# Optimization experiments

Hardware: AMD Instinct MI355X
Metric: run time of the kernel (lower is better)

The kernel has to match this reference:

```python
import jax, jax.numpy as jnp
import numpy as np

NHEAD = 8

def setup_inputs() -> dict:
    key = jax.random.key(0)
    k1, k2, k3, k4 = jax.random.split(key, 4)
    B, N, I, KQ, V = 2, 4096, 512, 512, 512
    x = jax.random.normal(k1, (B, N, I), dtype=jnp.float32)
    # store weights as [in, out] so projection is x @ W (same math as torch Linear with W.T)
    Wk = jax.random.normal(k2, (I, KQ), dtype=jnp.float32) * (1.0 / np.sqrt(I))
    Wq = jax.random.normal(k3, (I, KQ), dtype=jnp.float32) * (1.0 / np.sqrt(I))
    Wv = jax.random.normal(k4, (I, V), dtype=jnp.float32) * (1.0 / np.sqrt(I))
    return {"x": x, "Wk": Wk, "Wq": Wq, "Wv": Wv}

def reference(x, Wk, Wq, Wv):
    B, N, _ = x.shape
    H = NHEAD
    k = (x @ Wk).reshape(B, N, H, -1)   # [B,N,H,dk]
    q = (x @ Wq).reshape(B, N, H, -1)   # [B,N,H,dk]
    v = (x @ Wv).reshape(B, N, H, -1)   # [B,N,H,dv]
    dk = k.shape[-1]
    # scores[b,n,m,h] = k[b,n,h,:] . q[b,m,h,:] / sqrt(dk)
    scores = jnp.einsum('bnhd,bmhd->bnmh', k, q) / jnp.sqrt(jnp.asarray(dk, x.dtype))
    attn = jax.nn.softmax(scores, axis=-2)  # softmax over m (dim -2), matching torch code
    out = jnp.einsum('bnmh,bmhd->bnhd', attn, v)
    return out.reshape(B, N, -1)
```

## Files before the change

kernel.cpp:

```cpp
#include <hip/hip_runtime.h>
#include <hip/hip_bf16.h>

typedef __bf16 bf16_t;
typedef bf16_t bf16x8 __attribute__((ext_vector_type(8)));
typedef bf16_t bf16x4 __attribute__((ext_vector_type(4)));
typedef float f32x4 __attribute__((ext_vector_type(4)));

#define MFMA16(a, b, c) __builtin_amdgcn_mfma_f32_16x16x32_bf16(a, b, c, 0, 0, 0)

typedef __attribute__((address_space(3))) unsigned int lds_u32_t;
typedef __attribute__((address_space(1))) const unsigned int glb_u32_t;

__device__ __forceinline__ void gload16(const void* g, void* l) {
    __builtin_amdgcn_global_load_lds((glb_u32_t*)g, (lds_u32_t*)l, 16, 0, 0);
}

__device__ __forceinline__ bf16x8 lds8(const bf16_t* base, int row, int cb) {
    return *reinterpret_cast<const bf16x8*>(
        reinterpret_cast<const char*>(base) + row * 128 + (cb ^ ((row & 7) << 4)));
}

__global__ __launch_bounds__(256) void convert_x(
    const float* __restrict__ X, bf16_t* __restrict__ Xb)
{
    const size_t i = ((size_t)blockIdx.x * 256 + threadIdx.x) * 8;
    const float4 v0 = *reinterpret_cast<const float4*>(&X[i]);
    const float4 v1 = *reinterpret_cast<const float4*>(&X[i + 4]);
    bf16x8 o;
    o[0] = (bf16_t)v0.x; o[1] = (bf16_t)v0.y; o[2] = (bf16_t)v0.z; o[3] = (bf16_t)v0.w;
    o[4] = (bf16_t)v1.x; o[5] = (bf16_t)v1.y; o[6] = (bf16_t)v1.z; o[7] = (bf16_t)v1.w;
    *reinterpret_cast<bf16x8*>(&Xb[i]) = o;
}

__global__ __launch_bounds__(256) void transpose_w(
    const float* __restrict__ Wq, const float* __restrict__ Wk,
    const float* __restrict__ Wv, bf16_t* __restrict__ Wt)
{
    __shared__ float T[64][65];
    const int mat = blockIdx.z;
    const float* W = (mat == 0) ? Wq : (mat == 1 ? Wk : Wv);
    const int k0 = blockIdx.x * 64, n0 = blockIdx.y * 64;
    const int r = threadIdx.x >> 4, c4 = (threadIdx.x & 15) * 4;

    for (int rep = 0; rep < 4; ++rep) {
        const int row = r + rep * 16;
        const float4 v = *reinterpret_cast<const float4*>(&W[(size_t)(k0 + row) * 512 + n0 + c4]);
        T[row][c4 + 0] = v.x; T[row][c4 + 1] = v.y;
        T[row][c4 + 2] = v.z; T[row][c4 + 3] = v.w;
    }
    __syncthreads();
    const float scl = (mat == 1) ? 0.1803368801111204f : 1.0f;
    for (int rep = 0; rep < 4; ++rep) {
        const int nrow = r + rep * 16;
        bf16x4 o;
        for (int e = 0; e < 4; ++e) o[e] = (bf16_t)(T[c4 + e][nrow] * scl);
        *reinterpret_cast<bf16x4*>(&Wt[(size_t)mat * 262144 + (size_t)(n0 + nrow) * 512 + k0 + c4]) = o;
    }
}

__global__ __launch_bounds__(256, 2) void proj_bf16(
    const bf16_t* __restrict__ Xb, const bf16_t* __restrict__ Wt,
    bf16_t* __restrict__ Qb, bf16_t* __restrict__ Kb, bf16_t* __restrict__ Vt)
{
    __shared__ bf16_t Ab[2][128 * 64];
    __shared__ bf16_t Bb[2][128 * 64];

    const int tid = threadIdx.x;
    const int w = tid >> 6, l = tid & 63, g = l >> 4, lr = l & 15;
    const int m0 = blockIdx.x * 128;
    const int mat = blockIdx.y >> 2;
    const int n0 = (blockIdx.y & 3) * 128;
    const bf16_t* Wm = Wt + (size_t)mat * 262144;
    const int wm = (w >> 1) * 64, wn = (w & 1) * 64;

#define STAGE_P(buf, k0v)                                                   \
    do {                                                                    \
        for (int t = 0; t < 4; ++t) {                                       \
            const int rb = w * 32 + t * 8;                                  \
            const int row = rb + (l >> 3);                                  \
            const int cb = ((l & 7) << 4) ^ ((row & 7) << 4);               \
            gload16(&Xb[(size_t)(m0 + row) * 512 + (k0v) + (cb >> 1)],      \
                    &Ab[buf][rb * 64]);                                     \
            gload16(&Wm[(size_t)(n0 + row) * 512 + (k0v) + (cb >> 1)],      \
                    &Bb[buf][rb * 64]);                                     \
        }                                                                   \
    } while (0)

    f32x4 acc[4][4];
    const f32x4 z4 = {0.f, 0.f, 0.f, 0.f};
#pragma unroll
    for (int i = 0; i < 4; ++i)
#pragma unroll
        for (int j = 0; j < 4; ++j) acc[i][j] = z4;

    STAGE_P(0, 0);
    __syncthreads();

    for (int kk = 0; kk < 8; ++kk) {
        const int cur = kk & 1;
        if (kk + 1 < 8) STAGE_P(cur ^ 1, (kk + 1) * 64);

        bf16x8 a[4][2], bq[4][2];
#pragma unroll
        for (int fa = 0; fa < 4; ++fa)
#pragma unroll
            for (int dh = 0; dh < 2; ++dh) {
                a[fa][dh]  = lds8(Ab[cur], wm + fa * 16 + lr, dh * 64 + g * 16);
                bq[fa][dh] = lds8(Bb[cur], wn + fa * 16 + lr, dh * 64 + g * 16);
            }
        __builtin_amdgcn_s_setprio(1);
#pragma unroll
        for (int fa = 0; fa < 4; ++fa)
#pragma unroll
            for (int fb = 0; fb < 4; ++fb) {
                acc[fa][fb] = MFMA16(a[fa][0], bq[fb][0], acc[fa][fb]);
                acc[fa][fb] = MFMA16(a[fa][1], bq[fb][1], acc[fa][fb]);
            }
        __builtin_amdgcn_s_setprio(0);
        __syncthreads();
    }
#undef STAGE_P

#pragma unroll
    for (int fa = 0; fa < 4; ++fa)
#pragma unroll
        for (int fb = 0; fb < 4; ++fb)
#pragma unroll
            for (int j = 0; j < 4; ++j) {
                const int m = m0 + wm + fa * 16 + g * 4 + j;
                const int n = n0 + wn + fb * 16 + lr;
                const bf16_t val = (bf16_t)acc[fa][fb][j];
                if (mat == 0) {
                    Qb[(size_t)m * 512 + n] = val;
                } else if (mat == 1) {
                    Kb[(size_t)m * 512 + n] = val;
                } else {
                    const int b_ = m >> 12, mm = m & 4095;
                    const int hh = n >> 6, d = n & 63;
                    const int loc = mm & 63;
                    const int mperm = (mm & ~63) | (loc & 32) |
                                      (((loc >> 2) & 3) << 3) |
                                      (((loc >> 4) & 1) << 2) | (loc & 3);
                    Vt[((size_t)((b_ * 8 + hh) * 64 + d)) * 4096 + mperm] = val;
                }
            }
}

__global__ __launch_bounds__(256) void proj_kernel(
    const float* __restrict__ X,
    const float* __restrict__ Wq, const float* __restrict__ Wk,
    const float* __restrict__ Wv,
    bf16_t* __restrict__ Qb, bf16_t* __restrict__ Kb, bf16_t* __restrict__ Vt)
{
    __shared__ bf16_t Ax[128][40];
    __shared__ bf16_t Wtl[64][40];

    const int mode = blockIdx.z;
    const float* W = (mode == 0) ? Wq : (mode == 1 ? Wk : Wv);
    bf16_t* C = (mode == 0) ? Qb : (mode == 1 ? Kb : Vt);

    const int tid = threadIdx.x;
    const int w = tid >> 6, l = tid & 63, g = l >> 4, lr = l & 15;
    const int m0 = blockIdx.x * 128, n0 = blockIdx.y * 64;

    f32x4 acc[2][4];
    const f32x4 z4 = {0.f, 0.f, 0.f, 0.f};
    for (int i = 0; i < 2; ++i)
        for (int j = 0; j < 4; ++j) acc[i][j] = z4;

    for (int k0 = 0; k0 < 512; k0 += 32) {
        {
            const int c4 = (tid & 7) * 4;
            for (int r = 0; r < 4; ++r) {
                const int row = (tid >> 3) + r * 32;
                const float4 v = *reinterpret_cast<const float4*>(
                    &X[(size_t)(m0 + row) * 512 + k0 + c4]);
                bf16x4 o;
                o[0] = (bf16_t)v.x; o[1] = (bf16_t)v.y;
                o[2] = (bf16_t)v.z; o[3] = (bf16_t)v.w;
                *reinterpret_cast<bf16x4*>(&Ax[row][c4]) = o;
            }
        }
        {
            const int c4 = (tid & 15) * 4;
            for (int r = 0; r < 2; ++r) {
                const int krow = (tid >> 4) + r * 16;
                const float4 v = *reinterpret_cast<const float4*>(
                    &W[(size_t)(k0 + krow) * 512 + n0 + c4]);
                Wtl[c4 + 0][krow] = (bf16_t)v.x;
                Wtl[c4 + 1][krow] = (bf16_t)v.y;
                Wtl[c4 + 2][krow] = (bf16_t)v.z;
                Wtl[c4 + 3][krow] = (bf16_t)v.w;
            }
        }
        __syncthreads();

        bf16x8 a[2], bq[4];
        for (int fr = 0; fr < 2; ++fr)
            a[fr] = *reinterpret_cast<const bf16x8*>(&Ax[w * 32 + fr * 16 + lr][g * 8]);
        for (int fn = 0; fn < 4; ++fn)
            bq[fn] = *reinterpret_cast<const bf16x8*>(&Wtl[fn * 16 + lr][g * 8]);
        for (int fr = 0; fr < 2; ++fr)
            for (int fn = 0; fn < 4; ++fn)
                acc[fr][fn] = MFMA16(a[fr], bq[fn], acc[fr][fn]);
        __syncthreads();
    }

    const float SCL = 0.125f * 1.44269504088896f;
    for (int fr = 0; fr < 2; ++fr)
        for (int fn = 0; fn < 4; ++fn)
            for (int j = 0; j < 4; ++j) {
                const int m = m0 + w * 32 + fr * 16 + g * 4 + j;
                const int n = n0 + fn * 16 + lr;
                float vf = acc[fr][fn][j];
                if (mode == 1) vf *= SCL;
                const bf16_t val = (bf16_t)vf;
                if (mode <= 1) {
                    C[(size_t)m * 512 + n] = val;
                } else {
                    const int b_ = m >> 12, mm = m & 4095;
                    const int hh = n >> 6, d = n & 63;
                    const int loc = mm & 63;
                    const int mperm = (mm & ~63) | (loc & 32) |
                                      (((loc >> 2) & 3) << 3) |
                                      (((loc >> 4) & 1) << 2) | (loc & 3);
                    C[((size_t)((b_ * 8 + hh) * 64 + d)) * 4096 + mperm] = val;
                }
            }
}

__global__ __launch_bounds__(256, 2) void attn_kernel(
    const bf16_t* __restrict__ Kb, const bf16_t* __restrict__ Qb,
    const bf16_t* __restrict__ Vt, float* __restrict__ Out)
{
    __shared__ __align__(16) char smem[65536];

    const int tid = threadIdx.x;
    const int w = tid >> 6, l = tid & 63, g = l >> 4, lr = l & 15;
    const int mh = w >> 1, u = w & 1;
    const int bid = blockIdx.x;
    const int id = (bid & 7) * 64 + (bid >> 3);
    const int nb = id & 31, bh = id >> 5;
    const int b = bh >> 3, hd = bh & 7;
    const int n0 = nb * 128;

#define QL(buf) ((bf16_t*)(smem + mh * 16384 + (buf) * 8192))
#define VL(buf) ((bf16_t*)(smem + 32768 + mh * 16384 + (buf) * 8192))

    bf16x8 ak[4][2];
#pragma unroll
    for (int fr = 0; fr < 4; ++fr)
#pragma unroll
        for (int dh = 0; dh < 2; ++dh)
            ak[fr][dh] = *reinterpret_cast<const bf16x8*>(
                &Kb[(size_t)(b * 4096 + n0 + u * 64 + fr * 16 + lr) * 512 +
                    hd * 64 + dh * 32 + g * 8]);

    bf16x8 ones;
#pragma unroll
    for (int i = 0; i < 8; ++i) ones[i] = (bf16_t)1.0f;

#define STAGE(buf, m0v)                                                              \
    do {                                                                             \
        for (int t = 0; t < 4; ++t) {                                                \
            const int rb = u * 32 + t * 8;                                           \
            const int row = rb + (l >> 3);                                           \
            const int cb = ((l & 7) << 4) ^ ((row & 7) << 4);                        \
            gload16(&Qb[(size_t)(b * 4096 + (m0v) + row) * 512 + hd * 64 + (cb >> 1)],\
                    QL(buf) + rb * 64);                                              \
            gload16(&Vt[((size_t)(bh * 64 + row)) * 4096 + (m0v) + (cb >> 1)],       \
                    VL(buf) + rb * 64);                                              \
        }                                                                            \
    } while (0)

    f32x4 acc[4][4];
    f32x4 dacc[4];
    const f32x4 z4 = {0.f, 0.f, 0.f, 0.f};
#pragma unroll
    for (int fr = 0; fr < 4; ++fr) {
        dacc[fr] = z4;
#pragma unroll
        for (int j = 0; j < 4; ++j) acc[fr][j] = z4;
    }

    auto compute_tile = [&](int cur) {
        const bf16_t* qb = QL(cur);
        const bf16_t* vb = VL(cur);
        bf16x8 pa[4][2];
#pragma unroll
        for (int c = 0; c < 2; ++c) {
            f32x4 s[2][4];
#pragma unroll
            for (int mm = 0; mm < 2; ++mm)
#pragma unroll
                for (int fr = 0; fr < 4; ++fr) s[mm][fr] = z4;
            __builtin_amdgcn_s_setprio(1);
#pragma unroll
            for (int mm = 0; mm < 2; ++mm) {
                const int r = (c * 2 + mm) * 16 + lr;
                const bf16x8 a0 = lds8(qb, r, g * 16);
                const bf16x8 a1 = lds8(qb, r, 64 + g * 16);
#pragma unroll
                for (int fr = 0; fr < 4; ++fr) {
                    s[mm][fr] = MFMA16(a0, ak[fr][0], s[mm][fr]);
                    s[mm][fr] = MFMA16(a1, ak[fr][1], s[mm][fr]);
                }
            }
            __builtin_amdgcn_s_setprio(0);
#pragma unroll
            for (int fr = 0; fr < 4; ++fr)
#pragma unroll
                for (int e = 0; e < 8; ++e)
                    pa[fr][c][e] = (bf16_t)__builtin_amdgcn_exp2f(
                        s[e >> 2][fr][e & 3]);
        }
        __builtin_amdgcn_s_setprio(1);
#pragma unroll
        for (int fr = 0; fr < 4; ++fr) {
            dacc[fr] = MFMA16(pa[fr][0], ones, dacc[fr]);
            dacc[fr] = MFMA16(pa[fr][1], ones, dacc[fr]);
        }
#pragma unroll
        for (int fd = 0; fd < 4; ++fd) {
            const bf16x8 vb0 = lds8(vb, fd * 16 + lr, g * 16);
            const bf16x8 vb1 = lds8(vb, fd * 16 + lr, 64 + g * 16);
#pragma unroll
            for (int fr = 0; fr < 4; ++fr) {
                acc[fr][fd] = MFMA16(pa[fr][0], vb0, acc[fr][fd]);
                acc[fr][fd] = MFMA16(pa[fr][1], vb1, acc[fr][fd]);
            }
        }
        __builtin_amdgcn_s_setprio(0);
    };

    STAGE(0, mh * 2048);
    __syncthreads();

    for (int it = 0; it < 31; ++it) {
        STAGE((it + 1) & 1, (mh * 32 + it + 1) * 64);
        compute_tile(it & 1);
        __syncthreads();
    }
    compute_tile(1);
    __syncthreads();

    float* comb = (float*)smem;
    float* cden = (float*)(smem + 33280);
    if (mh == 1) {
#pragma unroll
        for (int fr = 0; fr < 4; ++fr)
#pragma unroll
            for (int fd = 0; fd < 4; ++fd)
#pragma unroll
                for (int j = 0; j < 4; ++j)
                    comb[(u * 64 + fr * 16 + g * 4 + j) * 65 + fd * 16 + lr] =
                        acc[fr][fd][j];
        if (lr == 0) {
#pragma unroll
            for (int fr = 0; fr < 4; ++fr)
#pragma unroll
                for (int j = 0; j < 4; ++j)
                    cden[u * 64 + fr * 16 + g * 4 + j] = dacc[fr][j];
        }
    }
    __syncthreads();
    if (mh == 0) {
        float linv[4][4];
#pragma unroll
        for (int fr = 0; fr < 4; ++fr)
#pragma unroll
            for (int j = 0; j < 4; ++j) {
                const int nl = u * 64 + fr * 16 + g * 4 + j;
                linv[fr][j] = 1.0f / (dacc[fr][j] + cden[nl]);
            }
#pragma unroll
        for (int fr = 0; fr < 4; ++fr)
#pragma unroll
            for (int fd = 0; fd < 4; ++fd)
#pragma unroll
                for (int j = 0; j < 4; ++j) {
                    const int nl = u * 64 + fr * 16 + g * 4 + j;
                    const int d = fd * 16 + lr;
                    Out[((size_t)(b * 4096 + n0 + nl)) * 512 + hd * 64 + d] =
                        (acc[fr][fd][j] + comb[nl * 65 + d]) * linv[fr][j];
                }
    }
#undef STAGE
#undef QL
#undef VL
}

extern "C" void kernel_launch(void* const* d_in, const int* in_sizes, int n_in,
                              void* d_out, int out_size, void* d_ws, size_t ws_size,
                              hipStream_t stream)
{
    const float* x  = (const float*)d_in[0];
    const float* Wk = (const float*)d_in[1];
    const float* Wq = (const float*)d_in[2];
    const float* Wv = (const float*)d_in[3];
    float* out = (float*)d_out;

    char* ws = (char*)d_ws;
    bf16_t* Kb = (bf16_t*)ws;
    bf16_t* Qb = Kb + (size_t)4194304;
    bf16_t* Vt = Qb + (size_t)4194304;
    bf16_t* Xb = (bf16_t*)(ws + 25165824);
    bf16_t* Wt = Xb + (size_t)4194304;

    const size_t NEED_PRE = 35127296;
    const bool has_pre = ws_size >= NEED_PRE;

    if (has_pre) {
        hipLaunchKernelGGL(convert_x, dim3(2048), dim3(256), 0, stream, x, Xb);
        hipLaunchKernelGGL(transpose_w, dim3(8, 8, 3), dim3(256), 0, stream,
                           Wq, Wk, Wv, Wt);
        hipLaunchKernelGGL(proj_bf16, dim3(64, 12), dim3(256), 0, stream,
                           Xb, Wt, Qb, Kb, Vt);
    } else {
        hipLaunchKernelGGL(proj_kernel, dim3(64, 8, 3), dim3(256), 0, stream,
                           x, Wq, Wk, Wv, Qb, Kb, Vt);
    }

    hipLaunchKernelGGL(attn_kernel, dim3(512), dim3(256), 0, stream,
                       Kb, Qb, Vt, out);
}
```

Baseline: 106.2 us.

## Split attention key range across blocks with fp16 partials and combine kernel

```diff
diff --git a/kernel.cpp b/kernel.cpp
--- a/kernel.cpp
+++ b/kernel.cpp
@@ -5,6 +5,7 @@
 typedef bf16_t bf16x8 __attribute__((ext_vector_type(8)));
 typedef bf16_t bf16x4 __attribute__((ext_vector_type(4)));
 typedef float f32x4 __attribute__((ext_vector_type(4)));
+typedef _Float16 f16x2 __attribute__((ext_vector_type(2)));
 
 #define MFMA16(a, b, c) __builtin_amdgcn_mfma_f32_16x16x32_bf16(a, b, c, 0, 0, 0)
 
@@ -229,23 +230,28 @@
             }
 }
 
-__global__ __launch_bounds__(256, 2) void attn_kernel(
+__global__ __launch_bounds__(256, 4) void attn_kernel(
     const bf16_t* __restrict__ Kb, const bf16_t* __restrict__ Qb,
-    const bf16_t* __restrict__ Vt, float* __restrict__ Out)
-{
-    __shared__ __align__(16) char smem[65536];
+    const bf16_t* __restrict__ Vt, float* __restrict__ Out,
+    _Float16* __restrict__ pO, float* __restrict__ pD, int nq)
+{
+    __shared__ __align__(16) char smem[32768];
 
     const int tid = threadIdx.x;
     const int w = tid >> 6, l = tid & 63, g = l >> 4, lr = l & 15;
-    const int mh = w >> 1, u = w & 1;
-    const int bid = blockIdx.x;
-    const int id = (bid & 7) * 64 + (bid >> 3);
-    const int nb = id & 31, bh = id >> 5;
+
+    const int nblk = 256 * nq, cpx = nblk >> 3;
+    const int id = (blockIdx.x & 7) * cpx + (blockIdx.x >> 3);
+    int bh, nb, q;
+    if (nq == 4) { bh = id >> 6; nb = (id >> 2) & 15; q = id & 3; }
+    else         { bh = id >> 4; nb = id & 15;        q = 0;     }
     const int b = bh >> 3, hd = bh & 7;
-    const int n0 = nb * 128;
-
-#define QL(buf) ((bf16_t*)(smem + mh * 16384 + (buf) * 8192))
-#define VL(buf) ((bf16_t*)(smem + 32768 + mh * 16384 + (buf) * 8192))
+    const int n0 = nb * 256;
+    const int ntiles = 64 / nq;
+    const int t0 = q * ntiles;
+
+#define QL(buf) ((bf16_t*)(smem + (buf) * 8192))
+#define VL(buf) ((bf16_t*)(smem + 16384 + (buf) * 8192))
 
     bf16x8 ak[4][2];
 #pragma unroll
@@ -253,7 +259,7 @@
 #pragma unroll
         for (int dh = 0; dh < 2; ++dh)
             ak[fr][dh] = *reinterpret_cast<const bf16x8*>(
-                &Kb[(size_t)(b * 4096 + n0 + u * 64 + fr * 16 + lr) * 512 +
+                &Kb[(size_t)(b * 4096 + n0 + w * 64 + fr * 16 + lr) * 512 +
                     hd * 64 + dh * 32 + g * 8]);
 
     bf16x8 ones;
@@ -262,8 +268,8 @@
 
 #define STAGE(buf, m0v)                                                              \
     do {                                                                             \
-        for (int t = 0; t < 4; ++t) {                                                \
-            const int rb = u * 32 + t * 8;                                           \
+        for (int t = 0; t < 2; ++t) {                                                \
+            const int rb = w * 16 + t * 8;                                           \
             const int row = rb + (l >> 3);                                           \
             const int cb = ((l & 7) << 4) ^ ((row & 7) << 4);                        \
             gload16(&Qb[(size_t)(b * 4096 + (m0v) + row) * 512 + hd * 64 + (cb >> 1)],\
@@ -333,61 +339,80 @@
         __builtin_amdgcn_s_setprio(0);
     };
 
-    STAGE(0, mh * 2048);
+    STAGE(0, t0 * 64);
     __syncthreads();
 
-    for (int it = 0; it < 31; ++it) {
-        STAGE((it + 1) & 1, (mh * 32 + it + 1) * 64);
+    for (int it = 0; it < ntiles - 1; ++it) {
+        STAGE((it + 1) & 1, (t0 + it + 1) * 64);
         compute_tile(it & 1);
         __syncthreads();
     }
-    compute_tile(1);
-    __syncthreads();
-
-    float* comb = (float*)smem;
-    float* cden = (float*)(smem + 33280);
-    if (mh == 1) {
+    compute_tile((ntiles - 1) & 1);
+
+    if (nq == 1) {
+        float linv[4][4];
 #pragma unroll
         for (int fr = 0; fr < 4; ++fr)
 #pragma unroll
+            for (int j = 0; j < 4; ++j) linv[fr][j] = 1.0f / dacc[fr][j];
+#pragma unroll
+        for (int fr = 0; fr < 4; ++fr)
+#pragma unroll
             for (int fd = 0; fd < 4; ++fd)
 #pragma unroll
-                for (int j = 0; j < 4; ++j)
-                    comb[(u * 64 + fr * 16 + g * 4 + j) * 65 + fd * 16 + lr] =
-                        acc[fr][fd][j];
+                for (int j = 0; j < 4; ++j) {
+                    const int n = n0 + w * 64 + fr * 16 + g * 4 + j;
+                    Out[((size_t)(b * 4096 + n)) * 512 + hd * 64 + fd * 16 + lr] =
+                        acc[fr][fd][j] * linv[fr][j];
+                }
+    } else {
+        const size_t qb_ = ((size_t)(q * 16 + bh)) << 18;
+#pragma unroll
+        for (int fr = 0; fr < 4; ++fr)
+#pragma unroll
+            for (int fd = 0; fd < 4; ++fd)
+#pragma unroll
+                for (int j = 0; j < 4; ++j) {
+                    const int n = n0 + w * 64 + fr * 16 + g * 4 + j;
+                    pO[qb_ + ((size_t)n << 6) + fd * 16 + lr] = (_Float16)acc[fr][fd][j];
+                }
         if (lr == 0) {
 #pragma unroll
             for (int fr = 0; fr < 4; ++fr)
 #pragma unroll
-                for (int j = 0; j < 4; ++j)
-                    cden[u * 64 + fr * 16 + g * 4 + j] = dacc[fr][j];
-        }
-    }
-    __syncthreads();
-    if (mh == 0) {
-        float linv[4][4];
-#pragma unroll
-        for (int fr = 0; fr < 4; ++fr)
-#pragma unroll
-            for (int j = 0; j < 4; ++j) {
-                const int nl = u * 64 + fr * 16 + g * 4 + j;
-                linv[fr][j] = 1.0f / (dacc[fr][j] + cden[nl]);
-            }
-#pragma unroll
-        for (int fr = 0; fr < 4; ++fr)
-#pragma unroll
-            for (int fd = 0; fd < 4; ++fd)
-#pragma unroll
                 for (int j = 0; j < 4; ++j) {
-                    const int nl = u * 64 + fr * 16 + g * 4 + j;
-                    const int d = fd * 16 + lr;
-                    Out[((size_t)(b * 4096 + n0 + nl)) * 512 + hd * 64 + d] =
-                        (acc[fr][fd][j] + comb[nl * 65 + d]) * linv[fr][j];
-                }
+                    const int n = n0 + w * 64 + fr * 16 + g * 4 + j;
+                    pD[(((size_t)(q * 16 + bh)) << 12) + n] = dacc[fr][j];
+                }
+        }
     }
 #undef STAGE
 #undef QL
 #undef VL
+}
+
+__global__ __launch_bounds__(256) void combine_kernel(
+    const _Float16* __restrict__ pO, const float* __restrict__ pD,
+    float* __restrict__ Out)
+{
+    const size_t i2 = ((size_t)blockIdx.x * 256 + threadIdx.x) * 2;
+    const int d = (int)(i2 & 63);
+    const int n = (int)((i2 >> 6) & 4095);
+    const int bh = (int)(i2 >> 18);
+
+    float s0 = 0.f, s1 = 0.f, den = 0.f;
+#pragma unroll
+    for (int q = 0; q < 4; ++q) {
+        const f16x2 v = *reinterpret_cast<const f16x2*>(
+            &pO[(((size_t)(q * 16 + bh)) << 18) + ((size_t)n << 6) + d]);
+        s0 += (float)v[0];
+        s1 += (float)v[1];
+        den += pD[(((size_t)(q * 16 + bh)) << 12) + n];
+    }
+    const float inv = 1.0f / den;
+    float2 o; o.x = s0 * inv; o.y = s1 * inv;
+    *reinterpret_cast<float2*>(
+        &Out[((size_t)((bh >> 3) * 4096 + n)) * 512 + (bh & 7) * 64 + d]) = o;
 }
 
 extern "C" void kernel_launch(void* const* d_in, const int* in_sizes, int n_in,
@@ -406,9 +431,13 @@
     bf16_t* Vt = Qb + (size_t)4194304;
     bf16_t* Xb = (bf16_t*)(ws + 25165824);
     bf16_t* Wt = Xb + (size_t)4194304;
-
-    const size_t NEED_PRE = 35127296;
-    const bool has_pre = ws_size >= NEED_PRE;
+    _Float16* pO = (_Float16*)(ws + 25165824);
+    float*    pD = (float*)(ws + 58720256);
+
+    const size_t NEED_PRE   = 35127296;
+    const size_t NEED_SPLIT = 59768832;
+    const bool has_pre   = ws_size >= NEED_PRE;
+    const bool has_split = ws_size >= NEED_SPLIT;
 
     if (has_pre) {
         hipLaunchKernelGGL(convert_x, dim3(2048), dim3(256), 0, stream, x, Xb);
@@ -421,6 +450,13 @@
                            x, Wq, Wk, Wv, Qb, Kb, Vt);
     }
 
-    hipLaunchKernelGGL(attn_kernel, dim3(512), dim3(256), 0, stream,
-                       Kb, Qb, Vt, out);
-}
+    if (has_split) {
+        hipLaunchKernelGGL(attn_kernel, dim3(1024), dim3(256), 0, stream,
+                           Kb, Qb, Vt, out, pO, pD, 4);
+        hipLaunchKernelGGL(combine_kernel, dim3(8192), dim3(256), 0, stream,
+                           pO, pD, out);
+    } else {
+        hipLaunchKernelGGL(attn_kernel, dim3(256), dim3(256), 0, stream,
+                           Kb, Qb, Vt, out, pO, pD, 1);
+    }
+}
```

After: 357.1 us. 3.36x slower.

## Split attention key range four ways in 1024-thread blocks covering 256 rows

Applied to the files above, without the earlier changes.

```diff
diff --git a/kernel.cpp b/kernel.cpp
--- a/kernel.cpp
+++ b/kernel.cpp
@@ -229,23 +229,22 @@
             }
 }
 
-__global__ __launch_bounds__(256, 2) void attn_kernel(
+__global__ __launch_bounds__(1024, 4) void attn_kernel(
     const bf16_t* __restrict__ Kb, const bf16_t* __restrict__ Qb,
     const bf16_t* __restrict__ Vt, float* __restrict__ Out)
 {
-    __shared__ __align__(16) char smem[65536];
+    __shared__ __align__(16) char smem[131072];
 
     const int tid = threadIdx.x;
     const int w = tid >> 6, l = tid & 63, g = l >> 4, lr = l & 15;
-    const int mh = w >> 1, u = w & 1;
-    const int bid = blockIdx.x;
-    const int id = (bid & 7) * 64 + (bid >> 3);
-    const int nb = id & 31, bh = id >> 5;
+    const int mh = w >> 2;
+    const int u = w & 3;
+
+    const int id = ((int)blockIdx.x & 7) * 32 + ((int)blockIdx.x >> 3);
+    const int bh = id >> 4, nb = id & 15;
     const int b = bh >> 3, hd = bh & 7;
-    const int n0 = nb * 128;
-
-#define QL(buf) ((bf16_t*)(smem + mh * 16384 + (buf) * 8192))
-#define VL(buf) ((bf16_t*)(smem + 32768 + mh * 16384 + (buf) * 8192))
+    const int n0 = nb * 256;
+    const int t0 = mh * 16;
 
     bf16x8 ak[4][2];
 #pragma unroll
@@ -262,14 +261,16 @@
 
 #define STAGE(buf, m0v)                                                              \
     do {                                                                             \
-        for (int t = 0; t < 4; ++t) {                                                \
-            const int rb = u * 32 + t * 8;                                           \
+        char* qls = smem + mh * 32768 + (buf) * 16384;                               \
+        char* vls = qls + 8192;                                                      \
+        for (int t = 0; t < 2; ++t) {                                                \
+            const int rb = u * 16 + t * 8;                                           \
             const int row = rb + (l >> 3);                                           \
             const int cb = ((l & 7) << 4) ^ ((row & 7) << 4);                        \
             gload16(&Qb[(size_t)(b * 4096 + (m0v) + row) * 512 + hd * 64 + (cb >> 1)],\
-                    QL(buf) + rb * 64);                                              \
+                    qls + rb * 128);                                                 \
             gload16(&Vt[((size_t)(bh * 64 + row)) * 4096 + (m0v) + (cb >> 1)],       \
-                    VL(buf) + rb * 64);                                              \
+                    vls + rb * 128);                                                 \
         }                                                                            \
     } while (0)
 
@@ -283,9 +284,9 @@
         for (int j = 0; j < 4; ++j) acc[fr][j] = z4;
     }
 
-    auto compute_tile = [&](int cur) {
-        const bf16_t* qb = QL(cur);
-        const bf16_t* vb = VL(cur);
+    auto compute_tile = [&](int buf) {
+        const bf16_t* qb = (const bf16_t*)(smem + mh * 32768 + buf * 16384);
+        const bf16_t* vb = (const bf16_t*)(smem + mh * 32768 + buf * 16384 + 8192);
         bf16x8 pa[4][2];
 #pragma unroll
         for (int c = 0; c < 2; ++c) {
@@ -333,36 +334,47 @@
         __builtin_amdgcn_s_setprio(0);
     };
 
-    STAGE(0, mh * 2048);
-    __syncthreads();
-
-    for (int it = 0; it < 31; ++it) {
-        STAGE((it + 1) & 1, (mh * 32 + it + 1) * 64);
+    STAGE(0, t0 * 64);
+    __syncthreads();
+
+    for (int it = 0; it < 16; ++it) {
+        if (it + 1 < 16) STAGE((it + 1) & 1, (t0 + it + 1) * 64);
         compute_tile(it & 1);
         __syncthreads();
     }
-    compute_tile(1);
-    __syncthreads();
 
     float* comb = (float*)smem;
-    float* cden = (float*)(smem + 33280);
-    if (mh == 1) {
-#pragma unroll
-        for (int fr = 0; fr < 4; ++fr)
-#pragma unroll
-            for (int fd = 0; fd < 4; ++fd)
-#pragma unroll
-                for (int j = 0; j < 4; ++j)
-                    comb[(u * 64 + fr * 16 + g * 4 + j) * 65 + fd * 16 + lr] =
-                        acc[fr][fd][j];
-        if (lr == 0) {
-#pragma unroll
-            for (int fr = 0; fr < 4; ++fr)
-#pragma unroll
-                for (int j = 0; j < 4; ++j)
-                    cden[u * 64 + fr * 16 + g * 4 + j] = dacc[fr][j];
-        }
-    }
+    float* cden = (float*)(smem + 66560);
+
+#define DUMP(ADD)                                                            \
+    do {                                                                     \
+        _Pragma("unroll")                                                    \
+        for (int fr = 0; fr < 4; ++fr)                                       \
+            _Pragma("unroll")                                                \
+            for (int fd = 0; fd < 4; ++fd)                                   \
+                _Pragma("unroll")                                            \
+                for (int j = 0; j < 4; ++j) {                                \
+                    const int nl = u * 64 + fr * 16 + g * 4 + j;             \
+                    float* p = &comb[nl * 65 + fd * 16 + lr];                \
+                    *p = (ADD ? *p : 0.f) + acc[fr][fd][j];                  \
+                }                                                            \
+        if (lr == 0) {                                                       \
+            _Pragma("unroll")                                                \
+            for (int fr = 0; fr < 4; ++fr)                                   \
+                _Pragma("unroll")                                            \
+                for (int j = 0; j < 4; ++j) {                                \
+                    const int nl = u * 64 + fr * 16 + g * 4 + j;             \
+                    float* p = &cden[nl];                                    \
+                    *p = (ADD ? *p : 0.f) + dacc[fr][j];                     \
+                }                                                            \
+        }                                                                    \
+    } while (0)
+
+    if (mh == 1) DUMP(0);
+    __syncthreads();
+    if (mh == 2) DUMP(1);
+    __syncthreads();
+    if (mh == 3) DUMP(1);
     __syncthreads();
     if (mh == 0) {
         float linv[4][4];
@@ -385,9 +397,8 @@
                         (acc[fr][fd][j] + comb[nl * 65 + d]) * linv[fr][j];
                 }
     }
+#undef DUMP
 #undef STAGE
-#undef QL
-#undef VL
 }
 
 extern "C" void kernel_launch(void* const* d_in, const int* in_sizes, int n_in,
@@ -421,6 +432,6 @@
                            x, Wq, Wk, Wv, Qb, Kb, Vt);
     }
 
-    hipLaunchKernelGGL(attn_kernel, dim3(512), dim3(256), 0, stream,
+    hipLaunchKernelGGL(attn_kernel, dim3(256), dim3(1024), 0, stream,
                        Kb, Qb, Vt, out);
 }
```

Result: slower. 349.4 us (+229.0%).

## Split attention block across eight waves with 32 query rows each

Applied to the files above, without the earlier changes.

```diff
diff --git a/kernel.cpp b/kernel.cpp
--- a/kernel.cpp
+++ b/kernel.cpp
@@ -229,7 +229,7 @@
             }
 }
 
-__global__ __launch_bounds__(256, 2) void attn_kernel(
+__global__ __launch_bounds__(512, 2) void attn_kernel(
     const bf16_t* __restrict__ Kb, const bf16_t* __restrict__ Qb,
     const bf16_t* __restrict__ Vt, float* __restrict__ Out)
 {
@@ -237,23 +237,22 @@
 
     const int tid = threadIdx.x;
     const int w = tid >> 6, l = tid & 63, g = l >> 4, lr = l & 15;
-    const int mh = w >> 1, u = w & 1;
-    const int bid = blockIdx.x;
-    const int id = (bid & 7) * 64 + (bid >> 3);
-    const int nb = id & 31, bh = id >> 5;
+    const int mh = w >> 2;
+    const int u = w & 3;
+
+    const int id = ((int)blockIdx.x & 7) * 64 + ((int)blockIdx.x >> 3);
+    const int bh = id >> 5, nb = id & 31;
     const int b = bh >> 3, hd = bh & 7;
     const int n0 = nb * 128;
-
-#define QL(buf) ((bf16_t*)(smem + mh * 16384 + (buf) * 8192))
-#define VL(buf) ((bf16_t*)(smem + 32768 + mh * 16384 + (buf) * 8192))
-
-    bf16x8 ak[4][2];
-#pragma unroll
-    for (int fr = 0; fr < 4; ++fr)
+    const int t0 = mh * 32;
+
+    bf16x8 ak[2][2];
+#pragma unroll
+    for (int fr = 0; fr < 2; ++fr)
 #pragma unroll
         for (int dh = 0; dh < 2; ++dh)
             ak[fr][dh] = *reinterpret_cast<const bf16x8*>(
-                &Kb[(size_t)(b * 4096 + n0 + u * 64 + fr * 16 + lr) * 512 +
+                &Kb[(size_t)(b * 4096 + n0 + u * 32 + fr * 16 + lr) * 512 +
                     hd * 64 + dh * 32 + g * 8]);
 
     bf16x8 ones;
@@ -262,132 +261,131 @@
 
 #define STAGE(buf, m0v)                                                              \
     do {                                                                             \
-        for (int t = 0; t < 4; ++t) {                                                \
-            const int rb = u * 32 + t * 8;                                           \
+        char* qls = smem + mh * 32768 + (buf) * 16384;                               \
+        char* vls = qls + 8192;                                                      \
+        for (int t = 0; t < 2; ++t) {                                                \
+            const int rb = u * 16 + t * 8;                                           \
             const int row = rb + (l >> 3);                                           \
             const int cb = ((l & 7) << 4) ^ ((row & 7) << 4);                        \
             gload16(&Qb[(size_t)(b * 4096 + (m0v) + row) * 512 + hd * 64 + (cb >> 1)],\
-                    QL(buf) + rb * 64);                                              \
+                    qls + rb * 128);                                                 \
             gload16(&Vt[((size_t)(bh * 64 + row)) * 4096 + (m0v) + (cb >> 1)],       \
-                    VL(buf) + rb * 64);                                              \
+                    vls + rb * 128);                                                 \
         }                                                                            \
     } while (0)
 
-    f32x4 acc[4][4];
-    f32x4 dacc[4];
+    f32x4 acc[2][4];
+    f32x4 dacc[2];
     const f32x4 z4 = {0.f, 0.f, 0.f, 0.f};
 #pragma unroll
-    for (int fr = 0; fr < 4; ++fr) {
+    for (int fr = 0; fr < 2; ++fr) {
         dacc[fr] = z4;
 #pragma unroll
         for (int j = 0; j < 4; ++j) acc[fr][j] = z4;
     }
 
-    auto compute_tile = [&](int cur) {
-        const bf16_t* qb = QL(cur);
-        const bf16_t* vb = VL(cur);
-        bf16x8 pa[4][2];
-#pragma unroll
-        for (int c = 0; c < 2; ++c) {
-            f32x4 s[2][4];
-#pragma unroll
-            for (int mm = 0; mm < 2; ++mm)
-#pragma unroll
-                for (int fr = 0; fr < 4; ++fr) s[mm][fr] = z4;
-            __builtin_amdgcn_s_setprio(1);
-#pragma unroll
-            for (int mm = 0; mm < 2; ++mm) {
-                const int r = (c * 2 + mm) * 16 + lr;
-                const bf16x8 a0 = lds8(qb, r, g * 16);
-                const bf16x8 a1 = lds8(qb, r, 64 + g * 16);
-#pragma unroll
-                for (int fr = 0; fr < 4; ++fr) {
-                    s[mm][fr] = MFMA16(a0, ak[fr][0], s[mm][fr]);
-                    s[mm][fr] = MFMA16(a1, ak[fr][1], s[mm][fr]);
-                }
-            }
-            __builtin_amdgcn_s_setprio(0);
-#pragma unroll
-            for (int fr = 0; fr < 4; ++fr)
+    auto compute_tile = [&](int buf) {
+        const bf16_t* qb = (const bf16_t*)(smem + mh * 32768 + buf * 16384);
+        const bf16_t* vb = (const bf16_t*)(smem + mh * 32768 + buf * 16384 + 8192);
+
+        f32x4 s[4][2];
+#pragma unroll
+        for (int m16 = 0; m16 < 4; ++m16)
+#pragma unroll
+            for (int fr = 0; fr < 2; ++fr) s[m16][fr] = z4;
+
+        __builtin_amdgcn_s_setprio(1);
+#pragma unroll
+        for (int m16 = 0; m16 < 4; ++m16) {
+            const int r = m16 * 16 + lr;
+            const bf16x8 a0 = lds8(qb, r, g * 16);
+            const bf16x8 a1 = lds8(qb, r, 64 + g * 16);
+            s[m16][0] = MFMA16(a0, ak[0][0], s[m16][0]);
+            s[m16][0] = MFMA16(a1, ak[0][1], s[m16][0]);
+            s[m16][1] = MFMA16(a0, ak[1][0], s[m16][1]);
+            s[m16][1] = MFMA16(a1, ak[1][1], s[m16][1]);
+        }
+        __builtin_amdgcn_s_setprio(0);
+
+        bf16x8 pa[2][2];
+#pragma unroll
+        for (int fr = 0; fr < 2; ++fr)
+#pragma unroll
+            for (int c = 0; c < 2; ++c)
 #pragma unroll
                 for (int e = 0; e < 8; ++e)
                     pa[fr][c][e] = (bf16_t)__builtin_amdgcn_exp2f(
-                        s[e >> 2][fr][e & 3]);
-        }
+                        s[c * 2 + (e >> 2)][fr][e & 3]);
+
         __builtin_amdgcn_s_setprio(1);
-#pragma unroll
-        for (int fr = 0; fr < 4; ++fr) {
-            dacc[fr] = MFMA16(pa[fr][0], ones, dacc[fr]);
-            dacc[fr] = MFMA16(pa[fr][1], ones, dacc[fr]);
-        }
+        dacc[0] = MFMA16(pa[0][0], ones, dacc[0]);
+        dacc[0] = MFMA16(pa[0][1], ones, dacc[0]);
+        dacc[1] = MFMA16(pa[1][0], ones, dacc[1]);
+        dacc[1] = MFMA16(pa[1][1], ones, dacc[1]);
 #pragma unroll
         for (int fd = 0; fd < 4; ++fd) {
             const bf16x8 vb0 = lds8(vb, fd * 16 + lr, g * 16);
             const bf16x8 vb1 = lds8(vb, fd * 16 + lr, 64 + g * 16);
-#pragma unroll
-            for (int fr = 0; fr < 4; ++fr) {
-                acc[fr][fd] = MFMA16(pa[fr][0], vb0, acc[fr][fd]);
-                acc[fr][fd] = MFMA16(pa[fr][1], vb1, acc[fr][fd]);
-            }
+            acc[0][fd] = MFMA16(pa[0][0], vb0, acc[0][fd]);
+            acc[0][fd] = MFMA16(pa[0][1], vb1, acc[0][fd]);
+            acc[1][fd] = MFMA16(pa[1][0], vb0, acc[1][fd]);
+            acc[1][fd] = MFMA16(pa[1][1], vb1, acc[1][fd]);
         }
         __builtin_amdgcn_s_setprio(0);
     };
 
-    STAGE(0, mh * 2048);
+    STAGE(0, t0 * 64);
     __syncthreads();
 
-    for (int it = 0; it < 31; ++it) {
-        STAGE((it + 1) & 1, (mh * 32 + it + 1) * 64);
+    for (int it = 0; it < 32; ++it) {
+        if (it + 1 < 32) STAGE((it + 1) & 1, (t0 + it + 1) * 64);
         compute_tile(it & 1);
         __syncthreads();
     }
-    compute_tile(1);
-    __syncthreads();
 
     float* comb = (float*)smem;
     float* cden = (float*)(smem + 33280);
+
     if (mh == 1) {
 #pragma unroll
-        for (int fr = 0; fr < 4; ++fr)
+        for (int fr = 0; fr < 2; ++fr)
 #pragma unroll
             for (int fd = 0; fd < 4; ++fd)
 #pragma unroll
                 for (int j = 0; j < 4; ++j)
-                    comb[(u * 64 + fr * 16 + g * 4 + j) * 65 + fd * 16 + lr] =
+                    comb[(u * 32 + fr * 16 + g * 4 + j) * 65 + fd * 16 + lr] =
                         acc[fr][fd][j];
         if (lr == 0) {
 #pragma unroll
-            for (int fr = 0; fr < 4; ++fr)
+            for (int fr = 0; fr < 2; ++fr)
 #pragma unroll
                 for (int j = 0; j < 4; ++j)
-                    cden[u * 64 + fr * 16 + g * 4 + j] = dacc[fr][j];
+                    cden[u * 32 + fr * 16 + g * 4 + j] = dacc[fr][j];
         }
     }
     __syncthreads();
     if (mh == 0) {
-        float linv[4][4];
-#pragma unroll
-        for (int fr = 0; fr < 4; ++fr)
+        float linv[2][4];
+#pragma unroll
+        for (int fr = 0; fr < 2; ++fr)
 #pragma unroll
             for (int j = 0; j < 4; ++j) {
-                const int nl = u * 64 + fr * 16 + g * 4 + j;
+                const int nl = u * 32 + fr * 16 + g * 4 + j;
                 linv[fr][j] = 1.0f / (dacc[fr][j] + cden[nl]);
             }
 #pragma unroll
-        for (int fr = 0; fr < 4; ++fr)
+        for (int fr = 0; fr < 2; ++fr)
 #pragma unroll
             for (int fd = 0; fd < 4; ++fd)
 #pragma unroll
                 for (int j = 0; j < 4; ++j) {
-                    const int nl = u * 64 + fr * 16 + g * 4 + j;
+                    const int nl = u * 32 + fr * 16 + g * 4 + j;
                     const int d = fd * 16 + lr;
                     Out[((size_t)(b * 4096 + n0 + nl)) * 512 + hd * 64 + d] =
                         (acc[fr][fd][j] + comb[nl * 65 + d]) * linv[fr][j];
                 }
     }
 #undef STAGE
-#undef QL
-#undef VL
 }
 
 extern "C" void kernel_launch(void* const* d_in, const int* in_sizes, int n_in,
@@ -421,6 +419,6 @@
                            x, Wq, Wk, Wv, Qb, Kb, Vt);
     }
 
-    hipLaunchKernelGGL(attn_kernel, dim3(512), dim3(256), 0, stream,
+    hipLaunchKernelGGL(attn_kernel, dim3(512), dim3(512), 0, stream,
                        Kb, Qb, Vt, out);
 }
```

New measurement: 104.2 us. Within noise of the previous version (-1.9%).
